# Performance work log

Measured on AMD Instinct MI355X. Metric: run time of the kernel, lower is better.

Reference implementation:

```python
import jax, jax.numpy as jnp
import numpy as np

B, CIN, H, W = 32, 64, 112, 112
COUT, KH, KW = 64, 3, 3
STRIDE = (1, 1)
PADDING = ((1, 1), (1, 1))
DILATION = (1, 1)


def setup_inputs() -> dict:
    key = jax.random.key(0)
    k1, k2, k3 = jax.random.split(key, 3)
    # quantized activations and weights, int8 value range [-128, 127]
    x_q = jax.random.randint(k1, (B, CIN, H, W), -128, 128, dtype=jnp.int32).astype(jnp.int8)
    w_q = jax.random.randint(k2, (COUT, CIN, KH, KW), -128, 128, dtype=jnp.int32).astype(jnp.int8)
    weight_scale = jnp.float32(0.02)   # per-tensor weight scale
    act_scale = jnp.float32(0.05)      # per-tensor activation scale
    bias = jax.random.normal(k3, (COUT,), dtype=jnp.float32)
    return {"x_q": x_q, "w_q": w_q, "weight_scale": weight_scale,
            "act_scale": act_scale, "bias": bias}


def reference(x_q, w_q, weight_scale, act_scale, bias):
    acc = jax.lax.conv_general_dilated(
        x_q.astype(jnp.int32), w_q.astype(jnp.int32),
        window_strides=STRIDE, padding=PADDING, rhs_dilation=DILATION,
        dimension_numbers=("NCHW", "OIHW", "NCHW"),
        preferred_element_type=jnp.int32)
    # fused dequant (per-tensor scales) + FP32 bias -> FP32 output [B, COUT, H, W]
    out = acc.astype(jnp.float32) * (act_scale * weight_scale) + bias[None, :, None, None]
    return out
```

## Files before the change

### kernel.cpp

```cpp
#include <hip/hip_runtime.h>
#include <stdint.h>

#define BATCH 32
#define CIN   64
#define HH    112
#define WW    112
#define COUT_ 64

typedef int v4i __attribute__((ext_vector_type(4)));

__global__ void wtrans_kernel(const int* __restrict__ wq, int8_t* __restrict__ wt) {
    int idx = blockIdx.x * 256 + threadIdx.x;
    int ci   = idx & 63;
    int khkw = (idx >> 6) % 9;
    int co   = idx / 576;
    wt[idx] = (int8_t)wq[co * 576 + ci * 9 + khkw];
}

__launch_bounds__(256, 2)
__global__ void conv_kernel(const int* __restrict__ x,
                            const int8_t* __restrict__ wt,
                            const float*  __restrict__ wscale,
                            const float*  __restrict__ ascale,
                            const float*  __restrict__ bias,
                            float*        __restrict__ out) {
    __shared__ int8_t xs[4 * 114 * 72];

    const int tid = threadIdx.x;
    const int bt  = blockIdx.x;
    const int b   = bt / 56;
    const int h0  = (bt % 56) * 2;

    #pragma unroll
    for (int it = 0; it < 7; ++it) {
        int job = tid + it * 256;
        int ci4 = job & 15;
        int cg  = (job >> 4) % 28;
        int row = job / 448;
        int hh  = h0 - 1 + row;
        v4i q0 = {0,0,0,0}, q1 = {0,0,0,0}, q2 = {0,0,0,0}, q3 = {0,0,0,0};
        if (hh >= 0 && hh < HH) {
            const v4i* gp = (const v4i*)
                (x + ((size_t)(b * CIN + ci4 * 4) * HH + hh) * WW + cg * 4);
            q0 = gp[0];
            q1 = gp[3136];
            q2 = gp[2 * 3136];
            q3 = gp[3 * 3136];
        }
        #pragma unroll
        for (int j = 0; j < 4; ++j) {
            uint32_t lo01 = __builtin_amdgcn_perm((uint32_t)q1[j], (uint32_t)q0[j], 0x0C0C0400u);
            uint32_t lo23 = __builtin_amdgcn_perm((uint32_t)q3[j], (uint32_t)q2[j], 0x04000C0Cu);
            int addr = (row * 114 + cg * 4 + 1 + j) * 72 + ci4 * 4;
            *(uint32_t*)&xs[addr] = lo01 | lo23;
        }
    }
    if (tid < 128) {
        int ci4 = tid & 15;
        int col = ((tid >> 4) & 1) ? 113 : 0;
        int row = tid >> 5;
        *(uint32_t*)&xs[(row * 114 + col) * 72 + ci4 * 4] = 0u;
    }
    __syncthreads();

    const int lane = tid & 63;
    const int wave = tid >> 6;
    const int ln15 = lane & 15;
    const int quad = lane >> 4;
    const int r    = wave >> 1;
    const int coh  = wave & 1;
    const int cobase = coh * 32;

    v4i acc[2][7];
    #pragma unroll
    for (int mt = 0; mt < 2; ++mt)
        #pragma unroll
        for (int nt = 0; nt < 7; ++nt)
            acc[mt][nt] = (v4i){0, 0, 0, 0};

    const long* w64a = (const long*)(wt + (size_t)(cobase + ln15) * 576);
    const long* w64b = (const long*)(wt + (size_t)(cobase + 16 + ln15) * 576);

    #pragma unroll
    for (int kc = 0; kc < 18; ++kc) {
        const int khkw = kc >> 1;
        const int kh   = khkw / 3;
        const int kw   = khkw % 3;
        const int half = kc & 1;
        long a0 = w64a[kc * 4 + quad];
        long a1 = w64b[kc * 4 + quad];
        const int rowb  = (kh + r) * 114;
        const int cioff = half * 32 + quad * 8;
        #pragma unroll
        for (int nt = 0; nt < 7; ++nt) {
            int col = nt * 16 + ln15 + kw;
            long bfrag = *(const long*)&xs[(rowb + col) * 72 + cioff];
            acc[0][nt] = __builtin_amdgcn_mfma_i32_16x16x32_i8(a0, bfrag, acc[0][nt], 0, 0, 0);
            acc[1][nt] = __builtin_amdgcn_mfma_i32_16x16x32_i8(a1, bfrag, acc[1][nt], 0, 0, 0);
        }
    }

    const float s = ascale[0] * wscale[0];
    const int h = h0 + r;
    #pragma unroll
    for (int mt = 0; mt < 2; ++mt) {
        #pragma unroll
        for (int reg = 0; reg < 4; ++reg) {
            int co = cobase + mt * 16 + quad * 4 + reg;
            float bv = bias[co];
            float* op = out + ((size_t)(b * COUT_ + co) * HH + h) * WW;
            #pragma unroll
            for (int nt = 0; nt < 7; ++nt) {
                int wp = nt * 16 + ln15;
                op[wp] = (float)acc[mt][nt][reg] * s + bv;
            }
        }
    }
}

extern "C" void kernel_launch(void* const* d_in, const int* in_sizes, int n_in,
                              void* d_out, int out_size, void* d_ws, size_t ws_size,
                              hipStream_t stream) {
    const int*    xq     = (const int*)d_in[0];
    const int*    wq     = (const int*)d_in[1];
    const float*  wscale = (const float*)d_in[2];
    const float*  ascale = (const float*)d_in[3];
    const float*  bias   = (const float*)d_in[4];
    int8_t* wt  = (int8_t*)d_ws;
    float*  out = (float*)d_out;

    wtrans_kernel<<<144, 256, 0, stream>>>(wq, wt);
    conv_kernel<<<BATCH * 56, 256, 0, stream>>>(xq, wt, wscale, ascale, bias, out);
}
```

Measured before the change: 212.9 us.

## Pre-repack input into padded int8 NHWC buffer and async-copy tiles to LDS

Adds a repack kernel that converts the int32 NCHW input into a zero-padded int8 channel-last buffer in workspace. The conv kernel then streams contiguous rows straight into LDS with global_load_lds and no per-element conversion, and its occupancy hint is raised. The aim is to remove the duplicated 4x-wide int32 reads and permutes done per block, since each input row was loaded by two blocks. The cost is an extra kernel launch and a round trip through the padded intermediate buffer. The old path is kept as a fallback for when the workspace is too small.

```diff
diff --git a/kernel.cpp b/kernel.cpp
--- a/kernel.cpp
+++ b/kernel.cpp
@@ -7,7 +7,18 @@
 #define WW    112
 #define COUT_ 64
 
+#define ROWB  8136
+#define IMGB  (114 * ROWB)
+#define XPAD_OFF 40960
+#define WS_REQ (XPAD_OFF + (size_t)BATCH * IMGB)
+
 typedef int v4i __attribute__((ext_vector_type(4)));
+
+__device__ inline void async_copy16(const void* g, void* l) {
+    __builtin_amdgcn_global_load_lds(
+        (const __attribute__((address_space(1))) uint8_t*)g,
+        (__attribute__((address_space(3))) uint8_t*)l, 16, 0, 0);
+}
 
 __global__ void wtrans_kernel(const int* __restrict__ wq, int8_t* __restrict__ wt) {
     int idx = blockIdx.x * 256 + threadIdx.x;
@@ -17,13 +28,133 @@
     wt[idx] = (int8_t)wq[co * 576 + ci * 9 + khkw];
 }
 
-__launch_bounds__(256, 2)
-__global__ void conv_kernel(const int* __restrict__ x,
+__global__ void repack_kernel(const int* __restrict__ x, int8_t* __restrict__ xp) {
+    const int tid = threadIdx.x;
+    const int b   = blockIdx.x / HH;
+    const int h   = blockIdx.x % HH;
+    int8_t* rowb = xp + (size_t)(b * 114 + h + 1) * ROWB;
+
+    #pragma unroll
+    for (int it = 0; it < 2; ++it) {
+        int job = tid + it * 256;
+        if (job < 448) {
+            int ci4 = job & 15;
+            int cg  = job >> 4;
+            const v4i* gp = (const v4i*)
+                (x + ((size_t)(b * CIN + ci4 * 4) * HH + h) * WW + cg * 4);
+            v4i q0 = gp[0];
+            v4i q1 = gp[3136];
+            v4i q2 = gp[2 * 3136];
+            v4i q3 = gp[3 * 3136];
+            #pragma unroll
+            for (int j = 0; j < 4; ++j) {
+                uint32_t lo01 = __builtin_amdgcn_perm((uint32_t)q1[j], (uint32_t)q0[j], 0x0C0C0400u);
+                uint32_t lo23 = __builtin_amdgcn_perm((uint32_t)q3[j], (uint32_t)q2[j], 0x04000C0Cu);
+                *(uint32_t*)&rowb[(cg * 4 + 1 + j) * 72 + ci4 * 4] = lo01 | lo23;
+            }
+        }
+    }
+    if (tid < 18) *(uint32_t*)&rowb[tid * 4] = 0u;
+    if (tid >= 32 && tid < 144) {
+        int wp = tid - 31;
+        *(uint64_t*)&rowb[wp * 72 + 64] = 0ull;
+    }
+    if (h == 0) {
+        int8_t* zr = xp + (size_t)(b * 114 + 0) * ROWB;
+        for (int i = tid; i < ROWB / 4; i += 256) *(uint32_t*)&zr[i * 4] = 0u;
+    }
+    if (h == HH - 1) {
+        int8_t* zr = xp + (size_t)(b * 114 + 113) * ROWB;
+        for (int i = tid; i < ROWB / 4; i += 256) *(uint32_t*)&zr[i * 4] = 0u;
+    }
+}
+
+__launch_bounds__(256, 5)
+__global__ void conv_kernel(const int8_t* __restrict__ xp,
                             const int8_t* __restrict__ wt,
                             const float*  __restrict__ wscale,
                             const float*  __restrict__ ascale,
                             const float*  __restrict__ bias,
                             float*        __restrict__ out) {
+    __shared__ int8_t xs[4 * ROWB + 72];
+
+    const int tid  = threadIdx.x;
+    const int lane = tid & 63;
+    const int wave = tid >> 6;
+    const int bt   = blockIdx.x;
+    const int b    = bt / 56;
+    const int h0   = (bt % 56) * 2;
+
+    const int8_t* gsrc = xp + (size_t)(b * 114 + h0) * ROWB;
+    #pragma unroll
+    for (int it = 0; it < 8; ++it) {
+        int chunk = it * 256 + tid;
+        if (chunk < 2034)
+            async_copy16(gsrc + (size_t)chunk * 16, xs + (it * 256 + wave * 64) * 16);
+    }
+    if (tid < 18) *(uint32_t*)&xs[4 * ROWB + tid * 4] = 0u;
+
+    const int ln15 = lane & 15;
+    const int quad = lane >> 4;
+    const int r    = wave >> 1;
+    const int coh  = wave & 1;
+    const int cobase = coh * 32;
+
+    v4i acc[2][7];
+    #pragma unroll
+    for (int mt = 0; mt < 2; ++mt)
+        #pragma unroll
+        for (int nt = 0; nt < 7; ++nt)
+            acc[mt][nt] = (v4i){0, 0, 0, 0};
+
+    const long* w64a = (const long*)(wt + (size_t)(cobase + ln15) * 576);
+    const long* w64b = (const long*)(wt + (size_t)(cobase + 16 + ln15) * 576);
+
+    __syncthreads();
+
+    #pragma unroll
+    for (int kc = 0; kc < 18; ++kc) {
+        const int khkw = kc >> 1;
+        const int kh   = khkw / 3;
+        const int kw   = khkw % 3;
+        const int half = kc & 1;
+        long a0 = w64a[kc * 4 + quad];
+        long a1 = w64b[kc * 4 + quad];
+        const int rb = (kh + r) * ROWB + half * 32 + quad * 8;
+        #pragma unroll
+        for (int nt = 0; nt < 7; ++nt) {
+            int col = nt * 16 + ln15 + kw;
+            long bfrag = *(const long*)&xs[rb + col * 72];
+            acc[0][nt] = __builtin_amdgcn_mfma_i32_16x16x32_i8(a0, bfrag, acc[0][nt], 0, 0, 0);
+            acc[1][nt] = __builtin_amdgcn_mfma_i32_16x16x32_i8(a1, bfrag, acc[1][nt], 0, 0, 0);
+        }
+    }
+
+    const float s = ascale[0] * wscale[0];
+    const int h = h0 + r;
+    #pragma unroll
+    for (int mt = 0; mt < 2; ++mt) {
+        #pragma unroll
+        for (int reg = 0; reg < 4; ++reg) {
+            int co = cobase + mt * 16 + quad * 4 + reg;
+            float bv = bias[co];
+            float* op = out + ((size_t)(b * COUT_ + co) * HH + h) * WW;
+            #pragma unroll
+            for (int nt = 0; nt < 7; ++nt) {
+                int wp = nt * 16 + ln15;
+                op[wp] = (float)acc[mt][nt][reg] * s + bv;
+            }
+        }
+    }
+}
+
+__launch_bounds__(256, 2)
+__global__ void conv_fb(const int* __restrict__ x,
+                        const int8_t* __restrict__ wt,
+                        const float*  __restrict__ wscale,
+                        const float*  __restrict__ ascale,
+                        const float*  __restrict__ bias,
+                        float*        __restrict__ out) {
     __shared__ int8_t xs[4 * 114 * 72];
 
     const int tid = threadIdx.x;
@@ -42,17 +173,13 @@
         if (hh >= 0 && hh < HH) {
             const v4i* gp = (const v4i*)
                 (x + ((size_t)(b * CIN + ci4 * 4) * HH + hh) * WW + cg * 4);
-            q0 = gp[0];
-            q1 = gp[3136];
-            q2 = gp[2 * 3136];
-            q3 = gp[3 * 3136];
+            q0 = gp[0]; q1 = gp[3136]; q2 = gp[2 * 3136]; q3 = gp[3 * 3136];
         }
         #pragma unroll
         for (int j = 0; j < 4; ++j) {
             uint32_t lo01 = __builtin_amdgcn_perm((uint32_t)q1[j], (uint32_t)q0[j], 0x0C0C0400u);
             uint32_t lo23 = __builtin_amdgcn_perm((uint32_t)q3[j], (uint32_t)q2[j], 0x04000C0Cu);
-            int addr = (row * 114 + cg * 4 + 1 + j) * 72 + ci4 * 4;
-            *(uint32_t*)&xs[addr] = lo01 | lo23;
+            *(uint32_t*)&xs[(row * 114 + cg * 4 + 1 + j) * 72 + ci4 * 4] = lo01 | lo23;
         }
     }
     if (tid < 128) {
@@ -130,5 +257,11 @@
     float*  out = (float*)d_out;
 
     wtrans_kernel<<<144, 256, 0, stream>>>(wq, wt);
-    conv_kernel<<<BATCH * 56, 256, 0, stream>>>(xq, wt, wscale, ascale, bias, out);
-}
+    if (ws_size >= WS_REQ) {
+        int8_t* xp = (int8_t*)d_ws + XPAD_OFF;
+        repack_kernel<<<BATCH * HH, 256, 0, stream>>>(xq, xp);
+        conv_kernel<<<BATCH * 56, 256, 0, stream>>>(xp, wt, wscale, ascale, bias, out);
+    } else {
+        conv_fb<<<BATCH * 56, 256, 0, stream>>>(xq, wt, wscale, ascale, bias, out);
+    }
+}
```

After: 277.7 us. 1.3x slower.
